# Performance work log

Hardware: AMD Instinct MI355X
Metric: run time of the kernel (lower is better)

Reference implementation:

```python
import jax, jax.numpy as jnp
import numpy as np

B, L = 128, 256          # trees per batch, leaves per tree (perfect binary tree)
V, D, H = 50000, 300, 512  # vocab, word_dim, tree_input_dim == output_dim


def setup_inputs() -> dict:
    key = jax.random.key(0)
    ks = jax.random.split(key, 6)
    token_ids = jax.random.randint(ks[0], (B, L), 0, V)
    scale_e = np.sqrt(3.0 / D).astype(np.float32)  # reset_embedding uniform(-scale, scale)
    emb_table = jax.random.uniform(ks[1], (V, D), jnp.float32, -scale_e, scale_e)
    s = 0.02
    Wx = jax.random.normal(ks[2], (D, 5 * H), jnp.float32) * s  # leaf input -> (i, fl, fr, o, u)
    Ul = jax.random.normal(ks[3], (H, 5 * H), jnp.float32) * s  # left child h
    Ur = jax.random.normal(ks[4], (H, 5 * H), jnp.float32) * s  # right child h
    b = jax.random.normal(ks[5], (5 * H,), jnp.float32) * s
    return {"token_ids": token_ids, "emb_table": emb_table, "Wx": Wx, "Ul": Ul, "Ur": Ur, "b": b}


def _cell(xproj, hl, hr, cl, cr, Ul, Ur, b):
    # Binary tree-LSTM cell (Tai et al., fold-style) with per-child forget gates.
    g = xproj + hl @ Ul + hr @ Ur + b            # [..., 5H]
    i, fl, fr, o, u = jnp.split(g, 5, axis=-1)
    c = jax.nn.sigmoid(i) * jnp.tanh(u) + jax.nn.sigmoid(fl) * cl + jax.nn.sigmoid(fr) * cr
    h = jax.nn.sigmoid(o) * jnp.tanh(c)
    return h, c


def reference(token_ids, emb_table, Wx, Ul, Ur, b):
    # Eval mode: all dropouts are identity.
    x = emb_table[token_ids]                      # [B, L, D] leaf word embeddings
    z = jnp.zeros((B, L, H), x.dtype)             # leaf children states are zero
    h, c = _cell(x @ Wx, z, z, z, z, Ul, Ur, b)   # all leaves at once
    hs = [h]
    # Level-wise bottom-up over the perfect binary tree (internal nodes: inputs=None).
    while h.shape[1] > 1:
        hl, hr = h[:, 0::2], h[:, 1::2]
        cl, cr = c[:, 0::2], c[:, 1::2]
        h, c = _cell(jnp.float32(0.0), hl, hr, cl, cr, Ul, Ur, b)
        hs.append(h)
    # Collected hidden states of all 2L-1 nodes (leaves first, then levels up to root).
    return jnp.concatenate(hs, axis=1)            # [B, 2L-1, H]
```

## Files before the change

kernel.cpp:

```cpp
#include <hip/hip_runtime.h>
#include <hip/hip_bf16.h>
#include <cstdint>

#define BB 128
#define LL 256
#define DD 300
#define HH 512
#define TOUT 511
#define NGATE 2560

typedef __attribute__((ext_vector_type(8))) short bf16x8;
typedef __attribute__((ext_vector_type(4))) float f32x4;

__device__ __forceinline__ float rcpf(float x){ return __builtin_amdgcn_rcpf(x); }
__device__ __forceinline__ float ex2f(float x){ return __builtin_amdgcn_exp2f(x); }
__device__ __forceinline__ float sigf(float x){ return rcpf(1.0f + ex2f(x * -1.44269504f)); }
__device__ __forceinline__ float tanh_fast(float x){ return 1.0f - 2.0f*rcpf(ex2f(x * 2.88539008f) + 1.0f); }

__device__ __forceinline__ void load_lds16(const void* g, void* l) {
  __builtin_amdgcn_global_load_lds(
      (const __attribute__((address_space(1))) unsigned int*)g,
      (__attribute__((address_space(3))) unsigned int*)l, 16, 0, 0);
}

#define VMWAIT(n) asm volatile("s_waitcnt vmcnt(" #n ")" ::: "memory")
#define LGKM0()   asm volatile("s_waitcnt lgkmcnt(0)" ::: "memory")

__global__ __launch_bounds__(256) void prep_weights(
    const float* __restrict__ Wx, const float* __restrict__ Ul, const float* __restrict__ Ur,
    __hip_bfloat16* __restrict__ Wb0t, __hip_bfloat16* __restrict__ Wb1t)
{
  const int z = blockIdx.z;
  const float* src; __hip_bfloat16* dst; int Ksrc, Kdst, koff;
  if (z == 0) { if (blockIdx.x >= 5) return; src = Wx; dst = Wb0t; Ksrc = DD; Kdst = 320; koff = 0; }
  else if (z == 1) { src = Ul; dst = Wb1t; Ksrc = HH; Kdst = 1024; koff = 0; }
  else { src = Ur; dst = Wb1t; Ksrc = HH; Kdst = 1024; koff = 512; }

  __shared__ float t[64][65];
  const int tid = threadIdx.x;
  const int k0 = blockIdx.x * 64;
  const int n0 = blockIdx.y * 64;
  #pragma unroll
  for (int p = 0; p < 16; ++p) {
    int lin = p*256 + tid;
    int ki = lin >> 6, nj = lin & 63;
    t[ki][nj] = (k0 + ki < Ksrc) ? src[(size_t)(k0+ki)*NGATE + n0 + nj] : 0.f;
  }
  __syncthreads();
  #pragma unroll
  for (int p = 0; p < 16; ++p) {
    int lin = p*256 + tid;
    int ni = lin >> 6, kj = lin & 63;
    dst[(size_t)(n0+ni)*Kdst + koff + k0 + kj] = __float2bfloat16(t[kj][ni]);
  }
}

__global__ void embed_cvt(const int* __restrict__ tok, const float* __restrict__ emb,
                          __hip_bfloat16* __restrict__ A0)
{
  int k = blockIdx.x * 64 + threadIdx.x;
  int r = blockIdx.y * 4 + threadIdx.y;
  int tk = tok[r];
  float v = (k < DD) ? emb[(size_t)tk*DD + k] : 0.f;
  A0[(size_t)r*320 + k] = __float2bfloat16(v);
}

__global__ __launch_bounds__(512, 2) void gemm_big(
    const __hip_bfloat16* __restrict__ A, const __hip_bfloat16* __restrict__ Wt,
    int K, const float* __restrict__ bias, const float* __restrict__ cprev,
    float* __restrict__ out, __hip_bfloat16* __restrict__ hout, float* __restrict__ cout,
    int lkshift, int sc)
{
  constexpr int HBYT = 36864;
  __shared__ __align__(16) char lds[4*HBYT];

  const int tid  = threadIdx.x;
  const int lane = tid & 63;
  const int wid  = tid >> 6;
  const int wm   = wid >> 2;
  const int wn   = wid & 3;
  const int bid  = blockIdx.x;
  const int m    = (bid & 7) + ((bid >> 6) << 3);
  const int s    = (bid >> 3) & 7;
  const int r0   = m * 256;
  const int n0   = s * 64;
  const size_t rowK = (size_t)K * 2;

  const int gi0 = (wid < 4) ? wid*5 : 20 + (wid-4)*4;
  const char* gsrc[5];
  #pragma unroll
  for (int i = 0; i < 5; ++i) {
    int gi = gi0 + i;
    if (gi < 16) {
      int row = gi*16 + (lane >> 2);
      int cs  = (lane & 3) ^ ((row >> 1) & 3);
      gsrc[i] = (const char*)A + (size_t)(r0 + row)*rowK + cs*16;
    } else {
      int rowb = (gi-16)*16 + (lane >> 2);
      int cs   = (lane & 3) ^ ((rowb >> 1) & 3);
      int grow = (rowb >> 6)*512 + n0 + (rowb & 63);
      gsrc[i] = (const char*)Wt + (size_t)grow*rowK + cs*16;
    }
  }
  const int ldst0 = gi0*1024 + lane*16;

  f32x4 acc[8][5];
  #pragma unroll
  for (int mf = 0; mf < 8; ++mf)
    #pragma unroll
    for (int g5 = 0; g5 < 5; ++g5)
      acc[mf][g5] = (f32x4){0.f,0.f,0.f,0.f};

  const int nt = K >> 5;
  auto stage = [&](int t){
    char* base = lds + (size_t)(t & 3)*HBYT + ldst0;
    const size_t kb = (size_t)t*64;
    if (wid < 4) {
      #pragma unroll
      for (int i = 0; i < 5; ++i) load_lds16(gsrc[i] + kb, base + i*1024);
    } else {
      #pragma unroll
      for (int i = 0; i < 4; ++i) load_lds16(gsrc[i] + kb, base + i*1024);
    }
  };

  stage(0); stage(1); stage(2);

  for (int t = 0; t < nt; ++t) {
    if (t + 2 < nt)      { if (wid < 4) VMWAIT(10); else VMWAIT(8); }
    else if (t + 1 < nt) { if (wid < 4) VMWAIT(5);  else VMWAIT(4); }
    else                 { VMWAIT(0); }
    LGKM0();
    __builtin_amdgcn_s_barrier();

    const char* Ab = lds + (size_t)(t & 3)*HBYT;
    const char* Bb = Ab + 16384;
    const int q = lane >> 4;

    bf16x8 b[5];
    #pragma unroll
    for (int g5 = 0; g5 < 5; ++g5) {
      int c = g5*64 + wn*16 + (lane & 15);
      b[g5] = *(const bf16x8*)(Bb + c*64 + ((q ^ ((c >> 1) & 3))*16));
    }
    bf16x8 a[4];
    #pragma unroll
    for (int i = 0; i < 4; ++i) {
      int r = wm*128 + i*16 + (lane & 15);
      a[i] = *(const bf16x8*)(Ab + r*64 + ((q ^ ((r >> 1) & 3))*16));
    }
    if (t + 3 < nt) stage(t + 3);
    __builtin_amdgcn_sched_barrier(0);
    __builtin_amdgcn_s_setprio(1);
    #pragma unroll
    for (int mf = 0; mf < 4; ++mf)
      #pragma unroll
      for (int g5 = 0; g5 < 5; ++g5)
        acc[mf][g5] = __builtin_amdgcn_mfma_f32_16x16x32_bf16(a[mf], b[g5], acc[mf][g5], 0, 0, 0);
    __builtin_amdgcn_s_setprio(0);

    #pragma unroll
    for (int i = 0; i < 4; ++i) {
      int r = wm*128 + (4+i)*16 + (lane & 15);
      a[i] = *(const bf16x8*)(Ab + r*64 + ((q ^ ((r >> 1) & 3))*16));
    }
    __builtin_amdgcn_sched_barrier(0);
    __builtin_amdgcn_s_setprio(1);
    #pragma unroll
    for (int mf = 0; mf < 4; ++mf)
      #pragma unroll
      for (int g5 = 0; g5 < 5; ++g5)
        acc[4+mf][g5] = __builtin_amdgcn_mfma_f32_16x16x32_bf16(a[mf], b[g5], acc[4+mf][g5], 0, 0, 0);
    __builtin_amdgcn_s_setprio(0);
  }

  const int Lmask = (1 << lkshift) - 1;
  const int jg = n0 + wn*16 + (lane & 15);
  float bia[5];
  #pragma unroll
  for (int g5 = 0; g5 < 5; ++g5) bia[g5] = bias[g5*HH + jg];
  #pragma unroll
  for (int mf = 0; mf < 8; ++mf) {
    #pragma unroll
    for (int v = 0; v < 4; ++v) {
      int rr = r0 + wm*128 + mf*16 + (lane >> 4)*4 + v;
      float gi  = acc[mf][0][v] + bia[0];
      float gfl = acc[mf][1][v] + bia[1];
      float gfr = acc[mf][2][v] + bia[2];
      float go  = acc[mf][3][v] + bia[3];
      float gu  = acc[mf][4][v] + bia[4];
      float cl = 0.f, cr = 0.f;
      if (cprev) {
        cl = cprev[(size_t)(2*rr)*HH + jg];
        cr = cprev[(size_t)(2*rr)*HH + HH + jg];
      }
      float cc = sigf(gi)*tanh_fast(gu) + sigf(gfl)*cl + sigf(gfr)*cr;
      float hh = sigf(go)*tanh_fast(cc);
      int b = rr >> lkshift;
      int t = rr & Lmask;
      out[((size_t)b*TOUT + sc + t)*HH + jg] = hh;
      hout[(size_t)rr*HH + jg] = __float2bfloat16(hh);
      cout[(size_t)rr*HH + jg] = cc;
    }
  }
}

__global__ __launch_bounds__(512, 2) void gemm_tail(
    const __hip_bfloat16* __restrict__ A, const __hip_bfloat16* __restrict__ Wt,
    const float* __restrict__ bias, const float* __restrict__ cprev,
    float* __restrict__ out, __hip_bfloat16* __restrict__ hout, float* __restrict__ cout,
    int lkshift, int sc, int numM)
{
  constexpr int ABYTES = 16384;
  constexpr int BUFS   = ABYTES + 40960;
  __shared__ __align__(16) char lds[2*BUFS];

  const int tid  = threadIdx.x;
  const int lane = tid & 63;
  const int wid  = tid >> 6;
  const int wm   = wid >> 2;
  const int wn   = wid & 3;
  const int bid  = blockIdx.x;
  int m, s;
  if (numM >= 8) { m = (bid & 7) + ((bid >> 6) << 3); s = (bid >> 3) & 7; }
  else           { m = bid % numM;  s = bid / numM; }
  const int r0   = m * 128;
  const int n0   = s * 64;
  constexpr size_t rowK = 2048;

  const int srow = lane >> 3;
  const int gq   = (lane & 7) ^ srow;
  const char* gsrc[7];
  #pragma unroll
  for (int ii = 0; ii < 7; ++ii) {
    int issue = wid*7 + ii;
    if (issue < 16) {
      int r = issue*8 + srow;
      gsrc[ii] = (const char*)A + (size_t)(r0 + r)*rowK + (size_t)gq*16;
    } else {
      int c = (issue-16)*8 + srow;
      int grow = (c >> 6)*512 + n0 + (c & 63);
      gsrc[ii] = (const char*)Wt + (size_t)grow*rowK + (size_t)gq*16;
    }
  }
  const int ldst0 = (wid*7)*1024 + lane*16;

  f32x4 acc[4][5];
  #pragma unroll
  for (int mf = 0; mf < 4; ++mf)
    #pragma unroll
    for (int g5 = 0; g5 < 5; ++g5)
      acc[mf][g5] = (f32x4){0.f,0.f,0.f,0.f};

  auto stage = [&](int buf, int kt){
    char* base = lds + buf*BUFS + ldst0;
    const size_t kb = (size_t)kt*128;
    #pragma unroll
    for (int ii = 0; ii < 7; ++ii) load_lds16(gsrc[ii] + kb, base + ii*1024);
  };

  stage(0, 0);
  int cur = 0;
  for (int kt = 0; kt < 16; ++kt) {
    if (kt + 1 < 16) {
      stage(cur ^ 1, kt + 1);
      VMWAIT(7);
    } else {
      VMWAIT(0);
    }
    __builtin_amdgcn_s_barrier();

    const char* Ab = lds + cur*BUFS;
    const char* Bb = Ab + ABYTES;
    #pragma unroll
    for (int s2 = 0; s2 < 2; ++s2) {
      const int qb = s2*4 + (lane >> 4);
      bf16x8 b[5];
      #pragma unroll
      for (int g5 = 0; g5 < 5; ++g5) {
        int c = g5*64 + wn*16 + (lane & 15);
        b[g5] = *(const bf16x8*)(Bb + c*128 + ((qb ^ (c & 7))*16));
      }
      __builtin_amdgcn_s_setprio(1);
      #pragma unroll
      for (int mf = 0; mf < 4; ++mf) {
        int r = wm*64 + mf*16 + (lane & 15);
        bf16x8 av = *(const bf16x8*)(Ab + r*128 + ((qb ^ (r & 7))*16));
        #pragma unroll
        for (int g5 = 0; g5 < 5; ++g5)
          acc[mf][g5] = __builtin_amdgcn_mfma_f32_16x16x32_bf16(av, b[g5], acc[mf][g5], 0, 0, 0);
      }
      __builtin_amdgcn_s_setprio(0);
    }
    __builtin_amdgcn_s_barrier();
    cur ^= 1;
  }

  const int Lmask = (1 << lkshift) - 1;
  const int jg = n0 + wn*16 + (lane & 15);
  float bia[5];
  #pragma unroll
  for (int g5 = 0; g5 < 5; ++g5) bia[g5] = bias[g5*HH + jg];
  #pragma unroll
  for (int mf = 0; mf < 4; ++mf) {
    #pragma unroll
    for (int v = 0; v < 4; ++v) {
      int rr = r0 + wm*64 + mf*16 + (lane >> 4)*4 + v;
      float gi  = acc[mf][0][v] + bia[0];
      float gfl = acc[mf][1][v] + bia[1];
      float gfr = acc[mf][2][v] + bia[2];
      float go  = acc[mf][3][v] + bia[3];
      float gu  = acc[mf][4][v] + bia[4];
      float cl = cprev[(size_t)(2*rr)*HH + jg];
      float cr = cprev[(size_t)(2*rr)*HH + HH + jg];
      float cc = sigf(gi)*tanh_fast(gu) + sigf(gfl)*cl + sigf(gfr)*cr;
      float hh = sigf(go)*tanh_fast(cc);
      int b = rr >> lkshift;
      int t = rr & Lmask;
      out[((size_t)b*TOUT + sc + t)*HH + jg] = hh;
      hout[(size_t)rr*HH + jg] = __float2bfloat16(hh);
      cout[(size_t)rr*HH + jg] = cc;
    }
  }
}

extern "C" void kernel_launch(void* const* d_in, const int* in_sizes, int n_in,
                              void* d_out, int out_size, void* d_ws, size_t ws_size,
                              hipStream_t stream) {
  (void)in_sizes; (void)n_in; (void)out_size; (void)ws_size;
  const int*   tok  = (const int*)d_in[0];
  const float* emb  = (const float*)d_in[1];
  const float* Wx   = (const float*)d_in[2];
  const float* Ul   = (const float*)d_in[3];
  const float* Ur   = (const float*)d_in[4];
  const float* bias = (const float*)d_in[5];
  float* out = (float*)d_out;

  char* ws = (char*)d_ws;
  size_t off = 0;
  __hip_bfloat16* Wb0t = (__hip_bfloat16*)(ws + off); off += (size_t)NGATE*320*2;
  __hip_bfloat16* Wb1t = (__hip_bfloat16*)(ws + off); off += (size_t)NGATE*1024*2;
  __hip_bfloat16* hA   = (__hip_bfloat16*)(ws + off); off += (size_t)32768*HH*2;
  __hip_bfloat16* hB   = (__hip_bfloat16*)(ws + off); off += (size_t)16384*HH*2;
  float*          cA   = (float*)(ws + off);          off += (size_t)32768*HH*4;
  float*          cB   = (float*)(ws + off);          off += (size_t)16384*HH*4;
  __hip_bfloat16* A0   = (__hip_bfloat16*)cB;

  prep_weights<<<dim3(8, 40, 3), 256, 0, stream>>>(Wx, Ul, Ur, Wb0t, Wb1t);
  embed_cvt<<<dim3(5, 8192), dim3(64,4), 0, stream>>>(tok, emb, A0);

  gemm_big<<<(32768/256)*8, 512, 0, stream>>>(A0, Wb0t, 320, bias, nullptr,
                                              out, hA, cA, 8, 0);
  gemm_big<<<(16384/256)*8, 512, 0, stream>>>(hA, Wb1t, 1024, bias, cA,
                                              out, hB, cB, 7, 256);
  gemm_big<<<(8192/256)*8, 512, 0, stream>>>(hB, Wb1t, 1024, bias, cB,
                                             out, hA, cA, 6, 384);
  for (int k = 3; k <= 8; ++k) {
    int M = 32768 >> k;
    int sc = HH - (HH >> k);
    const __hip_bfloat16* Ain = (k & 1) ? hA : hB;
    __hip_bfloat16*       hO  = (k & 1) ? hB : hA;
    const float*          cI  = (k & 1) ? cA : cB;
    float*                cO  = (k & 1) ? cB : cA;
    int numM = M / 128;
    gemm_tail<<<numM*8, 512, 0, stream>>>(Ain, Wb1t, bias, cI,
                                          out, hO, cO, 8 - k, sc, numM);
  }
}
```

Baseline: 441.9 us.

## Make gemm_big persistent over multiple row panels with a continuous prefetch pipeline

gemm_big now always launches 256 blocks, and each block loops over P consecutive 256-row panels (P=4, 2, 1 for the three big levels). The load pipeline carries across panel boundaries, so the next panel's tiles are prefetched while the current panel's epilogue runs, and accumulators are zeroed after each epilogue. The aim is one wave of blocks on the GPU instead of several partial waves, with amortized prologue and weight-tile reuse. The trade-off is longer serialized work per block and an epilogue that may stall the pipeline.

```diff
diff --git a/kernel.cpp b/kernel.cpp
--- a/kernel.cpp
+++ b/kernel.cpp
@@ -69,7 +69,7 @@
     const __hip_bfloat16* __restrict__ A, const __hip_bfloat16* __restrict__ Wt,
     int K, const float* __restrict__ bias, const float* __restrict__ cprev,
     float* __restrict__ out, __hip_bfloat16* __restrict__ hout, float* __restrict__ cout,
-    int lkshift, int sc)
+    int lkshift, int sc, int P)
 {
   constexpr int HBYT = 36864;
   __shared__ __align__(16) char lds[4*HBYT];
@@ -82,27 +82,51 @@
   const int bid  = blockIdx.x;
   const int m    = (bid & 7) + ((bid >> 6) << 3);
   const int s    = (bid >> 3) & 7;
-  const int r0   = m * 256;
   const int n0   = s * 64;
   const size_t rowK = (size_t)K * 2;
-
-  const int gi0 = (wid < 4) ? wid*5 : 20 + (wid-4)*4;
-  const char* gsrc[5];
+  const size_t panStride = 256 * rowK;
+
+  const int gi0  = (wid < 4) ? wid*5 : 20 + (wid-4)*4;
+  const int niss = (wid < 4) ? 5 : 4;
+  size_t aoffA[5];
+  const char* bsrc[5];
+  bool isA[5];
   #pragma unroll
   for (int i = 0; i < 5; ++i) {
     int gi = gi0 + i;
     if (gi < 16) {
       int row = gi*16 + (lane >> 2);
       int cs  = (lane & 3) ^ ((row >> 1) & 3);
-      gsrc[i] = (const char*)A + (size_t)(r0 + row)*rowK + cs*16;
+      isA[i] = true;  aoffA[i] = (size_t)row*rowK + cs*16;  bsrc[i] = nullptr;
     } else {
       int rowb = (gi-16)*16 + (lane >> 2);
       int cs   = (lane & 3) ^ ((rowb >> 1) & 3);
       int grow = (rowb >> 6)*512 + n0 + (rowb & 63);
-      gsrc[i] = (const char*)Wt + (size_t)grow*rowK + cs*16;
+      isA[i] = false; aoffA[i] = 0;  bsrc[i] = (const char*)Wt + (size_t)grow*rowK + cs*16;
     }
   }
   const int ldst0 = gi0*1024 + lane*16;
+
+  const int nt    = K >> 5;
+  const int total = P * nt;
+
+  int ts = 0;
+  int Tstage = 0;
+  const char* aPanStage = (const char*)A + (size_t)m * P * panStride;
+
+  auto stage = [&](){
+    char* base = lds + (size_t)(Tstage & 3)*HBYT + ldst0;
+    const size_t kb = (size_t)ts*64;
+    #pragma unroll
+    for (int i = 0; i < 5; ++i) {
+      if (i < niss) {
+        const char* g = isA[i] ? (aPanStage + aoffA[i] + kb) : (bsrc[i] + kb);
+        load_lds16(g, base + i*1024);
+      }
+    }
+    ++Tstage;
+    if (++ts == nt) { ts = 0; aPanStage += panStride; }
+  };
 
   f32x4 acc[8][5];
   #pragma unroll
@@ -111,96 +135,90 @@
     for (int g5 = 0; g5 < 5; ++g5)
       acc[mf][g5] = (f32x4){0.f,0.f,0.f,0.f};
 
-  const int nt = K >> 5;
-  auto stage = [&](int t){
-    char* base = lds + (size_t)(t & 3)*HBYT + ldst0;
-    const size_t kb = (size_t)t*64;
-    if (wid < 4) {
-      #pragma unroll
-      for (int i = 0; i < 5; ++i) load_lds16(gsrc[i] + kb, base + i*1024);
-    } else {
-      #pragma unroll
-      for (int i = 0; i < 4; ++i) load_lds16(gsrc[i] + kb, base + i*1024);
-    }
-  };
-
-  stage(0); stage(1); stage(2);
-
-  for (int t = 0; t < nt; ++t) {
-    if (t + 2 < nt)      { if (wid < 4) VMWAIT(10); else VMWAIT(8); }
-    else if (t + 1 < nt) { if (wid < 4) VMWAIT(5);  else VMWAIT(4); }
-    else                 { VMWAIT(0); }
-    LGKM0();
-    __builtin_amdgcn_s_barrier();
-
-    const char* Ab = lds + (size_t)(t & 3)*HBYT;
-    const char* Bb = Ab + 16384;
-    const int q = lane >> 4;
-
-    bf16x8 b[5];
-    #pragma unroll
-    for (int g5 = 0; g5 < 5; ++g5) {
-      int c = g5*64 + wn*16 + (lane & 15);
-      b[g5] = *(const bf16x8*)(Bb + c*64 + ((q ^ ((c >> 1) & 3))*16));
-    }
-    bf16x8 a[4];
-    #pragma unroll
-    for (int i = 0; i < 4; ++i) {
-      int r = wm*128 + i*16 + (lane & 15);
-      a[i] = *(const bf16x8*)(Ab + r*64 + ((q ^ ((r >> 1) & 3))*16));
-    }
-    if (t + 3 < nt) stage(t + 3);
-    __builtin_amdgcn_sched_barrier(0);
-    __builtin_amdgcn_s_setprio(1);
-    #pragma unroll
-    for (int mf = 0; mf < 4; ++mf)
-      #pragma unroll
-      for (int g5 = 0; g5 < 5; ++g5)
-        acc[mf][g5] = __builtin_amdgcn_mfma_f32_16x16x32_bf16(a[mf], b[g5], acc[mf][g5], 0, 0, 0);
-    __builtin_amdgcn_s_setprio(0);
-
-    #pragma unroll
-    for (int i = 0; i < 4; ++i) {
-      int r = wm*128 + (4+i)*16 + (lane & 15);
-      a[i] = *(const bf16x8*)(Ab + r*64 + ((q ^ ((r >> 1) & 3))*16));
-    }
-    __builtin_amdgcn_sched_barrier(0);
-    __builtin_amdgcn_s_setprio(1);
-    #pragma unroll
-    for (int mf = 0; mf < 4; ++mf)
-      #pragma unroll
-      for (int g5 = 0; g5 < 5; ++g5)
-        acc[4+mf][g5] = __builtin_amdgcn_mfma_f32_16x16x32_bf16(a[mf], b[g5], acc[4+mf][g5], 0, 0, 0);
-    __builtin_amdgcn_s_setprio(0);
-  }
-
-  const int Lmask = (1 << lkshift) - 1;
+  stage(); stage(); stage();
+
   const int jg = n0 + wn*16 + (lane & 15);
   float bia[5];
   #pragma unroll
   for (int g5 = 0; g5 < 5; ++g5) bia[g5] = bias[g5*HH + jg];
-  #pragma unroll
-  for (int mf = 0; mf < 8; ++mf) {
-    #pragma unroll
-    for (int v = 0; v < 4; ++v) {
-      int rr = r0 + wm*128 + mf*16 + (lane >> 4)*4 + v;
-      float gi  = acc[mf][0][v] + bia[0];
-      float gfl = acc[mf][1][v] + bia[1];
-      float gfr = acc[mf][2][v] + bia[2];
-      float go  = acc[mf][3][v] + bia[3];
-      float gu  = acc[mf][4][v] + bia[4];
-      float cl = 0.f, cr = 0.f;
-      if (cprev) {
-        cl = cprev[(size_t)(2*rr)*HH + jg];
-        cr = cprev[(size_t)(2*rr)*HH + HH + jg];
-      }
-      float cc = sigf(gi)*tanh_fast(gu) + sigf(gfl)*cl + sigf(gfr)*cr;
-      float hh = sigf(go)*tanh_fast(cc);
-      int b = rr >> lkshift;
-      int t = rr & Lmask;
-      out[((size_t)b*TOUT + sc + t)*HH + jg] = hh;
-      hout[(size_t)rr*HH + jg] = __float2bfloat16(hh);
-      cout[(size_t)rr*HH + jg] = cc;
+  const int Lmask = (1 << lkshift) - 1;
+
+  for (int p = 0; p < P; ++p) {
+    for (int t = 0; t < nt; ++t) {
+      const int Tc = p*nt + t;
+      if (Tc + 3 <= total)      { if (wid < 4) VMWAIT(10); else VMWAIT(8); }
+      else if (Tc + 2 <= total) { if (wid < 4) VMWAIT(5);  else VMWAIT(4); }
+      else                      { VMWAIT(0); }
+      LGKM0();
+      __builtin_amdgcn_s_barrier();
+
+      const char* Ab = lds + (size_t)(Tc & 3)*HBYT;
+      const char* Bb = Ab + 16384;
+      const int q = lane >> 4;
+
+      bf16x8 b[5];
+      #pragma unroll
+      for (int g5 = 0; g5 < 5; ++g5) {
+        int c = g5*64 + wn*16 + (lane & 15);
+        b[g5] = *(const bf16x8*)(Bb + c*64 + ((q ^ ((c >> 1) & 3))*16));
+      }
+      bf16x8 a[4];
+      #pragma unroll
+      for (int i = 0; i < 4; ++i) {
+        int r = wm*128 + i*16 + (lane & 15);
+        a[i] = *(const bf16x8*)(Ab + r*64 + ((q ^ ((r >> 1) & 3))*16));
+      }
+      if (Tstage < total) stage();
+      __builtin_amdgcn_sched_barrier(0);
+      __builtin_amdgcn_s_setprio(1);
+      #pragma unroll
+      for (int mf = 0; mf < 4; ++mf)
+        #pragma unroll
+        for (int g5 = 0; g5 < 5; ++g5)
+          acc[mf][g5] = __builtin_amdgcn_mfma_f32_16x16x32_bf16(a[mf], b[g5], acc[mf][g5], 0, 0, 0);
+      __builtin_amdgcn_s_setprio(0);
+
+      #pragma unroll
+      for (int i = 0; i < 4; ++i) {
+        int r = wm*128 + (4+i)*16 + (lane & 15);
+        a[i] = *(const bf16x8*)(Ab + r*64 + ((q ^ ((r >> 1) & 3))*16));
+      }
+      __builtin_amdgcn_sched_barrier(0);
+      __builtin_amdgcn_s_setprio(1);
+      #pragma unroll
+      for (int mf = 0; mf < 4; ++mf)
+        #pragma unroll
+        for (int g5 = 0; g5 < 5; ++g5)
+          acc[4+mf][g5] = __builtin_amdgcn_mfma_f32_16x16x32_bf16(a[mf], b[g5], acc[4+mf][g5], 0, 0, 0);
+      __builtin_amdgcn_s_setprio(0);
+    }
+
+    const int r0 = (m*P + p) * 256;
+    #pragma unroll
+    for (int mf = 0; mf < 8; ++mf) {
+      #pragma unroll
+      for (int v = 0; v < 4; ++v) {
+        int rr = r0 + wm*128 + mf*16 + (lane >> 4)*4 + v;
+        float gi  = acc[mf][0][v] + bia[0];
+        float gfl = acc[mf][1][v] + bia[1];
+        float gfr = acc[mf][2][v] + bia[2];
+        float go  = acc[mf][3][v] + bia[3];
+        float gu  = acc[mf][4][v] + bia[4];
+        float cl = 0.f, cr = 0.f;
+        if (cprev) {
+          cl = cprev[(size_t)(2*rr)*HH + jg];
+          cr = cprev[(size_t)(2*rr)*HH + HH + jg];
+        }
+        float cc = sigf(gi)*tanh_fast(gu) + sigf(gfl)*cl + sigf(gfr)*cr;
+        float hh = sigf(go)*tanh_fast(cc);
+        int b = rr >> lkshift;
+        int t2 = rr & Lmask;
+        out[((size_t)b*TOUT + sc + t2)*HH + jg] = hh;
+        hout[(size_t)rr*HH + jg] = __float2bfloat16(hh);
+        cout[(size_t)rr*HH + jg] = cc;
+        acc[mf][0][v]=0.f; acc[mf][1][v]=0.f; acc[mf][2][v]=0.f;
+        acc[mf][3][v]=0.f; acc[mf][4][v]=0.f;
+      }
     }
   }
 }
@@ -349,12 +367,12 @@
   prep_weights<<<dim3(8, 40, 3), 256, 0, stream>>>(Wx, Ul, Ur, Wb0t, Wb1t);
   embed_cvt<<<dim3(5, 8192), dim3(64,4), 0, stream>>>(tok, emb, A0);
 
-  gemm_big<<<(32768/256)*8, 512, 0, stream>>>(A0, Wb0t, 320, bias, nullptr,
-                                              out, hA, cA, 8, 0);
-  gemm_big<<<(16384/256)*8, 512, 0, stream>>>(hA, Wb1t, 1024, bias, cA,
-                                              out, hB, cB, 7, 256);
-  gemm_big<<<(8192/256)*8, 512, 0, stream>>>(hB, Wb1t, 1024, bias, cB,
-                                             out, hA, cA, 6, 384);
+  gemm_big<<<256, 512, 0, stream>>>(A0, Wb0t, 320, bias, nullptr,
+                                    out, hA, cA, 8, 0, 4);
+  gemm_big<<<256, 512, 0, stream>>>(hA, Wb1t, 1024, bias, cA,
+                                    out, hB, cB, 7, 256, 2);
+  gemm_big<<<256, 512, 0, stream>>>(hB, Wb1t, 1024, bias, cB,
+                                    out, hA, cA, 6, 384, 1);
   for (int k = 3; k <= 8; ++k) {
     int M = 32768 >> k;
     int sc = HH - (HH >> k);
```

New measurement: 448.4 us. About the same (+1.5%).

## Add dedicated leaf-level GEMM with persistent blocks looping over four M panels

Applied to the files above, without the earlier changes.

Replaces the generic gemm_big launch for the leaf level with a specialized gemm_l0 kernel. It uses 256 blocks, and each block processes four consecutive 256-row panels of the embedding matrix for its 64-column slice. The 4-stage LDS pipeline continues across panel boundaries instead of restarting per block. The leaf epilogue is simplified to skip the forget gates, since the child states are zero. This cuts block launch and pipeline prologue overhead and keeps weight tiles hot, at the cost of fewer blocks and less parallelism.

```diff
diff --git a/kernel.cpp b/kernel.cpp
--- a/kernel.cpp
+++ b/kernel.cpp
@@ -63,6 +63,164 @@
   int tk = tok[r];
   float v = (k < DD) ? emb[(size_t)tk*DD + k] : 0.f;
   A0[(size_t)r*320 + k] = __float2bfloat16(v);
+}
+
+__global__ __launch_bounds__(512, 2) void gemm_l0(
+    const __hip_bfloat16* __restrict__ A, const __hip_bfloat16* __restrict__ Wt,
+    const float* __restrict__ bias,
+    float* __restrict__ out, __hip_bfloat16* __restrict__ hout, float* __restrict__ cout)
+{
+  constexpr int P  = 4;
+  constexpr int NT = 10;
+  constexpr int HBYT = 36864;
+  constexpr size_t rowK = 640;
+  constexpr size_t panStride = 256 * rowK;
+  __shared__ __align__(16) char lds[4*HBYT];
+
+  const int tid  = threadIdx.x;
+  const int lane = tid & 63;
+  const int wid  = tid >> 6;
+  const int wm   = wid >> 2;
+  const int wn   = wid & 3;
+  const int bid  = blockIdx.x;
+  const int m    = (bid & 7) + ((bid >> 6) << 3);
+  const int s    = (bid >> 3) & 7;
+  const int n0   = s * 64;
+
+  const bool isAwave = (wid < 4);
+  const char* gsrc[5];
+  int ldst0;
+  if (isAwave) {
+    #pragma unroll
+    for (int i = 0; i < 4; ++i) {
+      int gi  = wid*4 + i;
+      int row = gi*16 + (lane >> 2);
+      int cs  = (lane & 3) ^ ((row >> 1) & 3);
+      gsrc[i] = (const char*)A + (size_t)m*P*panStride + (size_t)row*rowK + cs*16;
+    }
+    gsrc[4] = nullptr;
+    ldst0 = (wid*4)*1024 + lane*16;
+  } else {
+    #pragma unroll
+    for (int i = 0; i < 5; ++i) {
+      int bj   = (wid-4)*5 + i;
+      int rowb = bj*16 + (lane >> 2);
+      int cs   = (lane & 3) ^ ((rowb >> 1) & 3);
+      int grow = (rowb >> 6)*512 + n0 + (rowb & 63);
+      gsrc[i] = (const char*)Wt + (size_t)grow*rowK + cs*16;
+    }
+    ldst0 = 16384 + ((wid-4)*5)*1024 + lane*16;
+  }
+
+  f32x4 acc[8][5];
+  #pragma unroll
+  for (int mf = 0; mf < 8; ++mf)
+    #pragma unroll
+    for (int g5 = 0; g5 < 5; ++g5)
+      acc[mf][g5] = (f32x4){0.f,0.f,0.f,0.f};
+
+  int ts = 0, Tstage = 0;
+  auto stage = [&](){
+    char* base = lds + (size_t)(Tstage & 3)*HBYT + ldst0;
+    const size_t kb = (size_t)ts*64;
+    if (isAwave) {
+      #pragma unroll
+      for (int i = 0; i < 4; ++i) load_lds16(gsrc[i] + kb, base + i*1024);
+    } else {
+      #pragma unroll
+      for (int i = 0; i < 5; ++i) load_lds16(gsrc[i] + kb, base + i*1024);
+    }
+    ++Tstage;
+    if (++ts == NT) {
+      ts = 0;
+      if (isAwave) {
+        #pragma unroll
+        for (int i = 0; i < 4; ++i) gsrc[i] += panStride;
+      }
+    }
+  };
+
+  stage(); stage(); stage();
+
+  const int jg = n0 + wn*16 + (lane & 15);
+  float bia[5];
+  #pragma unroll
+  for (int g5 = 0; g5 < 5; ++g5) bia[g5] = bias[g5*HH + jg];
+
+  constexpr int total = P * NT;
+  #pragma unroll 1
+  for (int p = 0; p < P; ++p) {
+    #pragma unroll 1
+    for (int t = 0; t < NT; ++t) {
+      const int Tc = p*NT + t;
+      if (Tc + 3 <= total)      { if (isAwave) VMWAIT(8); else VMWAIT(10); }
+      else if (Tc + 2 <= total) { if (isAwave) VMWAIT(4); else VMWAIT(5); }
+      else                      { VMWAIT(0); }
+      LGKM0();
+      __builtin_amdgcn_s_barrier();
+
+      const char* Ab = lds + (size_t)(Tc & 3)*HBYT;
+      const char* Bb = Ab + 16384;
+      const int q = lane >> 4;
+
+      bf16x8 b[5];
+      #pragma unroll
+      for (int g5 = 0; g5 < 5; ++g5) {
+        int c = g5*64 + wn*16 + (lane & 15);
+        b[g5] = *(const bf16x8*)(Bb + c*64 + ((q ^ ((c >> 1) & 3))*16));
+      }
+      bf16x8 a[4];
+      #pragma unroll
+      for (int i = 0; i < 4; ++i) {
+        int r = wm*128 + i*16 + (lane & 15);
+        a[i] = *(const bf16x8*)(Ab + r*64 + ((q ^ ((r >> 1) & 3))*16));
+      }
+      if (Tstage < total) stage();
+      __builtin_amdgcn_sched_barrier(0);
+      __builtin_amdgcn_s_setprio(1);
+      #pragma unroll
+      for (int mf = 0; mf < 4; ++mf)
+        #pragma unroll
+        for (int g5 = 0; g5 < 5; ++g5)
+          acc[mf][g5] = __builtin_amdgcn_mfma_f32_16x16x32_bf16(a[mf], b[g5], acc[mf][g5], 0, 0, 0);
+      __builtin_amdgcn_s_setprio(0);
+
+      #pragma unroll
+      for (int i = 0; i < 4; ++i) {
+        int r = wm*128 + (4+i)*16 + (lane & 15);
+        a[i] = *(const bf16x8*)(Ab + r*64 + ((q ^ ((r >> 1) & 3))*16));
+      }
+      __builtin_amdgcn_sched_barrier(0);
+      __builtin_amdgcn_s_setprio(1);
+      #pragma unroll
+      for (int mf = 0; mf < 4; ++mf)
+        #pragma unroll
+        for (int g5 = 0; g5 < 5; ++g5)
+          acc[4+mf][g5] = __builtin_amdgcn_mfma_f32_16x16x32_bf16(a[mf], b[g5], acc[4+mf][g5], 0, 0, 0);
+      __builtin_amdgcn_s_setprio(0);
+    }
+
+    const int r0 = (m*P + p) * 256;
+    #pragma unroll
+    for (int mf = 0; mf < 8; ++mf) {
+      #pragma unroll
+      for (int v = 0; v < 4; ++v) {
+        int rr = r0 + wm*128 + mf*16 + (lane >> 4)*4 + v;
+        float gi  = acc[mf][0][v] + bia[0];
+        float go  = acc[mf][3][v] + bia[3];
+        float gu  = acc[mf][4][v] + bia[4];
+        float cc = sigf(gi)*tanh_fast(gu);
+        float hh = sigf(go)*tanh_fast(cc);
+        int b = rr >> 8;
+        int t2 = rr & 255;
+        out[((size_t)b*TOUT + t2)*HH + jg] = hh;
+        hout[(size_t)rr*HH + jg] = __float2bfloat16(hh);
+        cout[(size_t)rr*HH + jg] = cc;
+        acc[mf][0][v]=0.f; acc[mf][1][v]=0.f; acc[mf][2][v]=0.f;
+        acc[mf][3][v]=0.f; acc[mf][4][v]=0.f;
+      }
+    }
+  }
 }
 
 __global__ __launch_bounds__(512, 2) void gemm_big(
@@ -349,8 +507,7 @@
   prep_weights<<<dim3(8, 40, 3), 256, 0, stream>>>(Wx, Ul, Ur, Wb0t, Wb1t);
   embed_cvt<<<dim3(5, 8192), dim3(64,4), 0, stream>>>(tok, emb, A0);
 
-  gemm_big<<<(32768/256)*8, 512, 0, stream>>>(A0, Wb0t, 320, bias, nullptr,
-                                              out, hA, cA, 8, 0);
+  gemm_l0<<<256, 512, 0, stream>>>(A0, Wb0t, bias, out, hA, cA);
   gemm_big<<<(16384/256)*8, 512, 0, stream>>>(hA, Wb1t, 1024, bias, cA,
                                               out, hB, cB, 7, 256);
   gemm_big<<<(8192/256)*8, 512, 0, stream>>>(hB, Wb1t, 1024, bias, cB,
```

New measurement: 411.2 us. 1.07x faster.

## Make big GEMMs persistent over multiple panels with phase-split ring pipeline

Applied to the files above, without the earlier changes.

Replaces gemm_big with a templated gemm_ring4 kernel. It launches a fixed 256 blocks, and each block loops over P row panels so the 4-deep LDS ring keeps streaming across panel boundaries. Each K-step's loads are split into four phases interleaved with groups of MFMA work, and A and B loads are reassigned across the waves. The leaf level uses a HASC=false specialization that drops the forget-gate terms. The embedding gather is vectorized to 8 elements per thread. The aim is to cut per-block prologue and tail cost and smooth memory/compute overlap, at the cost of more barriers per K-step and fewer blocks for latency hiding.

```diff
diff --git a/kernel.cpp b/kernel.cpp
--- a/kernel.cpp
+++ b/kernel.cpp
@@ -55,23 +55,44 @@
   }
 }
 
-__global__ void embed_cvt(const int* __restrict__ tok, const float* __restrict__ emb,
-                          __hip_bfloat16* __restrict__ A0)
+__global__ __launch_bounds__(256) void embed_cvt(
+    const int* __restrict__ tok, const float* __restrict__ emb,
+    __hip_bfloat16* __restrict__ A0)
 {
-  int k = blockIdx.x * 64 + threadIdx.x;
-  int r = blockIdx.y * 4 + threadIdx.y;
+  int idx = blockIdx.x*256 + threadIdx.x;
+  int r  = idx / 40;
+  int ck = (idx - r*40) * 8;
   int tk = tok[r];
-  float v = (k < DD) ? emb[(size_t)tk*DD + k] : 0.f;
-  A0[(size_t)r*320 + k] = __float2bfloat16(v);
-}
-
-__global__ __launch_bounds__(512, 2) void gemm_big(
+  const float* erow = emb + (size_t)tk*DD;
+  float v[8];
+  if (ck + 8 <= DD) {
+    float4 lo = *reinterpret_cast<const float4*>(erow + ck);
+    float4 hi = *reinterpret_cast<const float4*>(erow + ck + 4);
+    v[0]=lo.x; v[1]=lo.y; v[2]=lo.z; v[3]=lo.w;
+    v[4]=hi.x; v[5]=hi.y; v[6]=hi.z; v[7]=hi.w;
+  } else {
+    #pragma unroll
+    for (int j = 0; j < 8; ++j) { int k = ck + j; v[j] = (k < DD) ? erow[k] : 0.f; }
+  }
+  bf16x8 o;
+  #pragma unroll
+  for (int j = 0; j < 8; ++j)
+    o[j] = (short)__bfloat16_as_ushort(__float2bfloat16(v[j]));
+  *reinterpret_cast<bf16x8*>(&A0[(size_t)r*320 + ck]) = o;
+}
+
+template<int KDIM, int P, bool HASC>
+__global__ __launch_bounds__(512, 2) void gemm_ring4(
     const __hip_bfloat16* __restrict__ A, const __hip_bfloat16* __restrict__ Wt,
-    int K, const float* __restrict__ bias, const float* __restrict__ cprev,
+    const float* __restrict__ bias, const float* __restrict__ cprev,
     float* __restrict__ out, __hip_bfloat16* __restrict__ hout, float* __restrict__ cout,
     int lkshift, int sc)
 {
+  constexpr int NT = KDIM >> 5;
   constexpr int HBYT = 36864;
+  constexpr size_t rowK = (size_t)KDIM * 2;
+  constexpr size_t panStride = 256 * rowK;
+  constexpr int total = P * NT;
   __shared__ __align__(16) char lds[4*HBYT];
 
   const int tid  = threadIdx.x;
@@ -82,27 +103,32 @@
   const int bid  = blockIdx.x;
   const int m    = (bid & 7) + ((bid >> 6) << 3);
   const int s    = (bid >> 3) & 7;
-  const int r0   = m * 256;
   const int n0   = s * 64;
-  const size_t rowK = (size_t)K * 2;
-
-  const int gi0 = (wid < 4) ? wid*5 : 20 + (wid-4)*4;
+
+  const bool isAwave = (wid < 4);
   const char* gsrc[5];
-  #pragma unroll
-  for (int i = 0; i < 5; ++i) {
-    int gi = gi0 + i;
-    if (gi < 16) {
+  int ldst0;
+  if (isAwave) {
+    #pragma unroll
+    for (int i = 0; i < 4; ++i) {
+      int gi  = wid*4 + i;
       int row = gi*16 + (lane >> 2);
       int cs  = (lane & 3) ^ ((row >> 1) & 3);
-      gsrc[i] = (const char*)A + (size_t)(r0 + row)*rowK + cs*16;
-    } else {
-      int rowb = (gi-16)*16 + (lane >> 2);
+      gsrc[i] = (const char*)A + (size_t)m*P*panStride + (size_t)row*rowK + cs*16;
+    }
+    gsrc[4] = nullptr;
+    ldst0 = (wid*4)*1024 + lane*16;
+  } else {
+    #pragma unroll
+    for (int i = 0; i < 5; ++i) {
+      int bj   = (wid-4)*5 + i;
+      int rowb = bj*16 + (lane >> 2);
       int cs   = (lane & 3) ^ ((rowb >> 1) & 3);
       int grow = (rowb >> 6)*512 + n0 + (rowb & 63);
       gsrc[i] = (const char*)Wt + (size_t)grow*rowK + cs*16;
     }
-  }
-  const int ldst0 = gi0*1024 + lane*16;
+    ldst0 = 16384 + ((wid-4)*5)*1024 + lane*16;
+  }
 
   f32x4 acc[8][5];
   #pragma unroll
@@ -111,96 +137,131 @@
     for (int g5 = 0; g5 < 5; ++g5)
       acc[mf][g5] = (f32x4){0.f,0.f,0.f,0.f};
 
-  const int nt = K >> 5;
-  auto stage = [&](int t){
-    char* base = lds + (size_t)(t & 3)*HBYT + ldst0;
-    const size_t kb = (size_t)t*64;
-    if (wid < 4) {
-      #pragma unroll
-      for (int i = 0; i < 5; ++i) load_lds16(gsrc[i] + kb, base + i*1024);
+  int ts = 0, Tstage = 0;
+  auto stagePhase = [&](int ph){
+    char* base = lds + (size_t)(Tstage & 3)*HBYT + ldst0;
+    const size_t kb = (size_t)ts*64;
+    if (isAwave) {
+      load_lds16(gsrc[ph] + kb, base + ph*1024);
     } else {
-      #pragma unroll
-      for (int i = 0; i < 4; ++i) load_lds16(gsrc[i] + kb, base + i*1024);
+      if (ph == 0) {
+        load_lds16(gsrc[0] + kb, base);
+        load_lds16(gsrc[1] + kb, base + 1024);
+      } else {
+        load_lds16(gsrc[ph+1] + kb, base + (ph+1)*1024);
+      }
+    }
+    if (ph == 3) {
+      ++Tstage;
+      if (++ts == NT) {
+        ts = 0;
+        if (isAwave) {
+          #pragma unroll
+          for (int i = 0; i < 4; ++i) gsrc[i] += panStride;
+        }
+      }
     }
   };
 
-  stage(0); stage(1); stage(2);
-
-  for (int t = 0; t < nt; ++t) {
-    if (t + 2 < nt)      { if (wid < 4) VMWAIT(10); else VMWAIT(8); }
-    else if (t + 1 < nt) { if (wid < 4) VMWAIT(5);  else VMWAIT(4); }
-    else                 { VMWAIT(0); }
-    LGKM0();
-    __builtin_amdgcn_s_barrier();
-
-    const char* Ab = lds + (size_t)(t & 3)*HBYT;
-    const char* Bb = Ab + 16384;
-    const int q = lane >> 4;
-
-    bf16x8 b[5];
-    #pragma unroll
-    for (int g5 = 0; g5 < 5; ++g5) {
-      int c = g5*64 + wn*16 + (lane & 15);
-      b[g5] = *(const bf16x8*)(Bb + c*64 + ((q ^ ((c >> 1) & 3))*16));
-    }
-    bf16x8 a[4];
-    #pragma unroll
-    for (int i = 0; i < 4; ++i) {
-      int r = wm*128 + i*16 + (lane & 15);
-      a[i] = *(const bf16x8*)(Ab + r*64 + ((q ^ ((r >> 1) & 3))*16));
-    }
-    if (t + 3 < nt) stage(t + 3);
-    __builtin_amdgcn_sched_barrier(0);
-    __builtin_amdgcn_s_setprio(1);
-    #pragma unroll
-    for (int mf = 0; mf < 4; ++mf)
-      #pragma unroll
-      for (int g5 = 0; g5 < 5; ++g5)
-        acc[mf][g5] = __builtin_amdgcn_mfma_f32_16x16x32_bf16(a[mf], b[g5], acc[mf][g5], 0, 0, 0);
-    __builtin_amdgcn_s_setprio(0);
-
-    #pragma unroll
-    for (int i = 0; i < 4; ++i) {
-      int r = wm*128 + (4+i)*16 + (lane & 15);
-      a[i] = *(const bf16x8*)(Ab + r*64 + ((q ^ ((r >> 1) & 3))*16));
-    }
-    __builtin_amdgcn_sched_barrier(0);
-    __builtin_amdgcn_s_setprio(1);
-    #pragma unroll
-    for (int mf = 0; mf < 4; ++mf)
-      #pragma unroll
-      for (int g5 = 0; g5 < 5; ++g5)
-        acc[4+mf][g5] = __builtin_amdgcn_mfma_f32_16x16x32_bf16(a[mf], b[g5], acc[4+mf][g5], 0, 0, 0);
-    __builtin_amdgcn_s_setprio(0);
-  }
-
-  const int Lmask = (1 << lkshift) - 1;
+  #pragma unroll
+  for (int pr = 0; pr < 3; ++pr)
+    #pragma unroll
+    for (int ph = 0; ph < 4; ++ph) stagePhase(ph);
+
   const int jg = n0 + wn*16 + (lane & 15);
   float bia[5];
   #pragma unroll
   for (int g5 = 0; g5 < 5; ++g5) bia[g5] = bias[g5*HH + jg];
-  #pragma unroll
-  for (int mf = 0; mf < 8; ++mf) {
-    #pragma unroll
-    for (int v = 0; v < 4; ++v) {
-      int rr = r0 + wm*128 + mf*16 + (lane >> 4)*4 + v;
-      float gi  = acc[mf][0][v] + bia[0];
-      float gfl = acc[mf][1][v] + bia[1];
-      float gfr = acc[mf][2][v] + bia[2];
-      float go  = acc[mf][3][v] + bia[3];
-      float gu  = acc[mf][4][v] + bia[4];
-      float cl = 0.f, cr = 0.f;
-      if (cprev) {
-        cl = cprev[(size_t)(2*rr)*HH + jg];
-        cr = cprev[(size_t)(2*rr)*HH + HH + jg];
-      }
-      float cc = sigf(gi)*tanh_fast(gu) + sigf(gfl)*cl + sigf(gfr)*cr;
-      float hh = sigf(go)*tanh_fast(cc);
-      int b = rr >> lkshift;
-      int t = rr & Lmask;
-      out[((size_t)b*TOUT + sc + t)*HH + jg] = hh;
-      hout[(size_t)rr*HH + jg] = __float2bfloat16(hh);
-      cout[(size_t)rr*HH + jg] = cc;
+
+  #pragma unroll 1
+  for (int p = 0; p < P; ++p) {
+    #pragma unroll 1
+    for (int t = 0; t < NT; ++t) {
+      const int Tc = p*NT + t;
+      const char* Ab = lds + (size_t)(Tc & 3)*HBYT;
+      const char* Bb = Ab + 16384;
+      const int q4 = lane >> 4;
+
+      if (Tc + 3 <= total)      { if (isAwave) VMWAIT(8); else VMWAIT(10); }
+      else if (Tc + 2 <= total) { if (isAwave) VMWAIT(4); else VMWAIT(5); }
+      else                      { VMWAIT(0); }
+      __builtin_amdgcn_s_barrier();
+
+      bf16x8 b[5];
+      {
+        #pragma unroll
+        for (int g5 = 0; g5 < 5; ++g5) {
+          int c = g5*64 + wn*16 + (lane & 15);
+          b[g5] = *(const bf16x8*)(Bb + c*64 + ((q4 ^ ((c >> 1) & 3))*16));
+        }
+        int r0r = wm*128 + (lane & 15);
+        bf16x8 a0 = *(const bf16x8*)(Ab + r0r*64 + ((q4 ^ ((r0r >> 1) & 3))*16));
+        int r1r = r0r + 16;
+        bf16x8 a1 = *(const bf16x8*)(Ab + r1r*64 + ((q4 ^ ((r1r >> 1) & 3))*16));
+        if (Tstage < total) stagePhase(0);
+        __builtin_amdgcn_s_barrier();
+        LGKM0(); __builtin_amdgcn_sched_barrier(0);
+        __builtin_amdgcn_s_setprio(1);
+        #pragma unroll
+        for (int g5 = 0; g5 < 5; ++g5)
+          acc[0][g5] = __builtin_amdgcn_mfma_f32_16x16x32_bf16(a0, b[g5], acc[0][g5], 0, 0, 0);
+        #pragma unroll
+        for (int g5 = 0; g5 < 5; ++g5)
+          acc[1][g5] = __builtin_amdgcn_mfma_f32_16x16x32_bf16(a1, b[g5], acc[1][g5], 0, 0, 0);
+        __builtin_amdgcn_s_setprio(0);
+        __builtin_amdgcn_s_barrier();
+      }
+
+      #pragma unroll
+      for (int ph = 1; ph < 4; ++ph) {
+        int r0r = wm*128 + (2*ph)*16 + (lane & 15);
+        bf16x8 a0 = *(const bf16x8*)(Ab + r0r*64 + ((q4 ^ ((r0r >> 1) & 3))*16));
+        int r1r = r0r + 16;
+        bf16x8 a1 = *(const bf16x8*)(Ab + r1r*64 + ((q4 ^ ((r1r >> 1) & 3))*16));
+        if (Tstage < total) stagePhase(ph);
+        __builtin_amdgcn_s_barrier();
+        LGKM0(); __builtin_amdgcn_sched_barrier(0);
+        __builtin_amdgcn_s_setprio(1);
+        #pragma unroll
+        for (int g5 = 0; g5 < 5; ++g5)
+          acc[2*ph][g5] = __builtin_amdgcn_mfma_f32_16x16x32_bf16(a0, b[g5], acc[2*ph][g5], 0, 0, 0);
+        #pragma unroll
+        for (int g5 = 0; g5 < 5; ++g5)
+          acc[2*ph+1][g5] = __builtin_amdgcn_mfma_f32_16x16x32_bf16(a1, b[g5], acc[2*ph+1][g5], 0, 0, 0);
+        __builtin_amdgcn_s_setprio(0);
+        __builtin_amdgcn_s_barrier();
+      }
+    }
+
+    const int r0 = (m*P + p) * 256;
+    const int Lmask = (1 << lkshift) - 1;
+    #pragma unroll
+    for (int mf = 0; mf < 8; ++mf) {
+      #pragma unroll
+      for (int v = 0; v < 4; ++v) {
+        int rr = r0 + wm*128 + mf*16 + (lane >> 4)*4 + v;
+        float gi  = acc[mf][0][v] + bia[0];
+        float go  = acc[mf][3][v] + bia[3];
+        float gu  = acc[mf][4][v] + bia[4];
+        float cc;
+        if (HASC) {
+          float gfl = acc[mf][1][v] + bia[1];
+          float gfr = acc[mf][2][v] + bia[2];
+          float cl = cprev[(size_t)(2*rr)*HH + jg];
+          float cr = cprev[(size_t)(2*rr)*HH + HH + jg];
+          cc = sigf(gi)*tanh_fast(gu) + sigf(gfl)*cl + sigf(gfr)*cr;
+        } else {
+          cc = sigf(gi)*tanh_fast(gu);
+        }
+        float hh = sigf(go)*tanh_fast(cc);
+        int b2 = rr >> lkshift;
+        int t2 = rr & Lmask;
+        out[((size_t)b2*TOUT + sc + t2)*HH + jg] = hh;
+        hout[(size_t)rr*HH + jg] = __float2bfloat16(hh);
+        cout[(size_t)rr*HH + jg] = cc;
+        acc[mf][0][v]=0.f; acc[mf][1][v]=0.f; acc[mf][2][v]=0.f;
+        acc[mf][3][v]=0.f; acc[mf][4][v]=0.f;
+      }
     }
   }
 }
@@ -347,14 +408,14 @@
   __hip_bfloat16* A0   = (__hip_bfloat16*)cB;
 
   prep_weights<<<dim3(8, 40, 3), 256, 0, stream>>>(Wx, Ul, Ur, Wb0t, Wb1t);
-  embed_cvt<<<dim3(5, 8192), dim3(64,4), 0, stream>>>(tok, emb, A0);
-
-  gemm_big<<<(32768/256)*8, 512, 0, stream>>>(A0, Wb0t, 320, bias, nullptr,
-                                              out, hA, cA, 8, 0);
-  gemm_big<<<(16384/256)*8, 512, 0, stream>>>(hA, Wb1t, 1024, bias, cA,
-                                              out, hB, cB, 7, 256);
-  gemm_big<<<(8192/256)*8, 512, 0, stream>>>(hB, Wb1t, 1024, bias, cB,
-                                             out, hA, cA, 6, 384);
+  embed_cvt<<<(32768*40)/256, 256, 0, stream>>>(tok, emb, A0);
+
+  gemm_ring4<320, 4, false><<<256, 512, 0, stream>>>(A0, Wb0t, bias, nullptr,
+                                                     out, hA, cA, 8, 0);
+  gemm_ring4<1024, 2, true><<<256, 512, 0, stream>>>(hA, Wb1t, bias, cA,
+                                                     out, hB, cB, 7, 256);
+  gemm_ring4<1024, 1, true><<<256, 512, 0, stream>>>(hB, Wb1t, bias, cB,
+                                                     out, hA, cA, 6, 384);
   for (int k = 3; k <= 8; ++k) {
     int M = 32768 >> k;
     int sc = HH - (HH >> k);
```

Result: slower. 493.8 us (+11.8%).
